# Optimization experiments

Measured on AMD Instinct MI355X. Metric: run time of the kernel, lower is better.

## Reference

```python
import jax, jax.numpy as jnp
import numpy as np

H = 12
PD = 4
DECAY = 0.99
OFFSETS = (1, 2, 4, 8)
_PI = np.array([0, 0, 0, 1, 1, 2])  # Plucker pair indices i for G(2,4)
_PJ = np.array([1, 2, 3, 2, 3, 3])  # Plucker pair indices j
_J6 = jnp.array([[0, 0, 0, 0, 0, 1], [0, 0, 0, 0, -1, 0], [0, 0, 0, 1, 0, 0],
                 [0, 0, 1, 0, 0, 0], [0, -1, 0, 0, 0, 0], [1, 0, 0, 0, 0, 0]],
                dtype=jnp.float32)


def exterior(p1, p2):
    # p1, p2: [..., 4] -> normalized Plucker coords [..., 6]
    L = p1[..., _PI] * p2[..., _PJ] - p1[..., _PJ] * p2[..., _PI]
    n = jnp.maximum(jnp.linalg.norm(L, axis=-1, keepdims=True), 1e-12)
    return L / n


def setup_inputs() -> dict:
    key = jax.random.key(0)
    ks = jax.random.split(key, 12)
    B, T, D = 2, 2048, 768
    s = 0.02
    return {
        "x": jax.random.normal(ks[0], (B, T, D), jnp.float32),
        "qkv_w": jax.random.normal(ks[1], (3 * D, D), jnp.float32) * s,
        "qkv_b": jnp.zeros((3 * D,), jnp.float32),
        "w1_write": jax.random.normal(ks[2], (PD * H, D), jnp.float32) * s,
        "w2_write": jax.random.normal(ks[3], (PD * H, D), jnp.float32) * s,
        "w1_read": jax.random.normal(ks[4], (PD * H, D), jnp.float32) * s,
        "w2_read": jax.random.normal(ks[5], (PD * H, D), jnp.float32) * s,
        "memv_w": jax.random.normal(ks[6], (D, D), jnp.float32) * s,
        "memv_b": jnp.zeros((D,), jnp.float32),
        "memg_w": jax.random.normal(ks[7], (H, D), jnp.float32) * s,
        "memg_b": jnp.zeros((H,), jnp.float32),
        "mem_scale": jnp.full((H,), 0.1, jnp.float32),
        "out_w": jax.random.normal(ks[8], (D, D), jnp.float32) * s,
        "out_b": jnp.zeros((D,), jnp.float32),
    }


def reference(x, qkv_w, qkv_b, w1_write, w2_write, w1_read, w2_read,
              memv_w, memv_b, memg_w, memg_b, mem_scale, out_w, out_b):
    B, T, D = x.shape
    dh = D // H
    scale = dh ** -0.5

    # --- standard causal attention (dropout disabled / eval mode) ---
    qkv = (x @ qkv_w.T + qkv_b).reshape(B, T, 3, H, dh)
    qkv = jnp.transpose(qkv, (2, 0, 3, 1, 4))  # [3,B,H,T,dh]
    q, k, v = qkv[0], qkv[1], qkv[2]
    att = jnp.einsum('bhtd,bhsd->bhts', q, k) * scale
    upper = jnp.triu(jnp.ones((T, T), bool), 1)
    att = jnp.where(upper, -jnp.inf, att)
    attn = jax.nn.softmax(att, axis=-1)
    seq_out = jnp.einsum('bhts,bhsd->bhtd', attn, v)
    seq_out = jnp.transpose(seq_out, (0, 2, 1, 3)).reshape(B, T, D)

    # --- multi-scale Plucker incidence memory ---
    r1 = (x @ w1_read.T).reshape(B, T, H, PD)
    r2 = (x @ w2_read.T).reshape(B, T, H, PD)
    read_h = jnp.transpose(exterior(r1, r2), (0, 2, 1, 3))  # [B,H,T,6]

    keep = jnp.tril(jnp.ones((T, T), bool), -1)  # strict lower triangle
    total = jnp.zeros((B, H, T, T), x.dtype)
    n_active = 0
    for off in OFFSETS:
        if off >= T:
            continue
        n_active += 1
        x_past = jnp.concatenate(
            [jnp.zeros((B, off, D), x.dtype), x[:, :-off]], axis=1)
        w1 = (x_past @ w1_write.T).reshape(B, T, H, PD)
        w2 = (x @ w2_write.T).reshape(B, T, H, PD)
        wl = exterior(w1, w2)                       # [B,T,H,6]
        jw = jnp.einsum('bthi,ij->bthj', wl, _J6)   # apply J
        jw = jnp.transpose(jw, (0, 2, 1, 3))        # [B,H,T,6]
        inc = jnp.einsum('bhtp,bhsp->bhts', read_h, jw)
        total = total + jnp.where(keep, inc * inc, 0.0)
    total = total / n_active

    pos = jnp.arange(T, dtype=x.dtype)
    decay_w = jnp.where(keep, DECAY ** (pos[:, None] - pos[None, :]), 0.0)
    total = total * decay_w
    mem_score = total.sum(axis=-1)  # [B,H,T]

    mem_val = x @ memv_w.T + memv_b
    gate = jax.nn.sigmoid(x @ memg_w.T + memg_b)  # [B,T,H]
    gated = jax.nn.sigmoid(jnp.transpose(mem_score, (0, 2, 1)) * mem_scale) * gate
    gated = gated.mean(axis=-1, keepdims=True)  # [B,T,1]

    return (seq_out + gated * mem_val) @ out_w.T + out_b
```

## Files before the change

### kernel.cpp

```cpp
#include <hip/hip_runtime.h>

#define H 12
#define T 2048
#define D 768
#define NBT 4096
#define SCALE 0.125f
#define DECAY_F 0.99f
#define NCHK 72
#define NBLK_ATTN (24 * NCHK)
#define NBLK_MS1 192

typedef __attribute__((ext_vector_type(8))) short bf16x8;
typedef __attribute__((ext_vector_type(4))) float f32x4;
typedef __attribute__((ext_vector_type(16))) float f32x16;

static __device__ __forceinline__ ushort f2bf(float f) {
  union { float f; unsigned u; } v; v.f = f;
  unsigned r = (v.u + 0x7FFFu + ((v.u >> 16) & 1u)) >> 16;
  return (ushort)r;
}
static __device__ __forceinline__ float bf2f(ushort u) {
  union { unsigned u; float f; } v; v.u = ((unsigned)u) << 16;
  return v.f;
}
static __device__ __forceinline__ unsigned cvtpk(float lo, float hi) {
  unsigned r;
  asm("v_cvt_pk_bf16_f32 %0, %1, %2" : "=v"(r) : "v"(lo), "v"(hi));
  return r;
}
static __device__ __forceinline__ void swap32(unsigned &a, unsigned &b) {
  asm("v_permlane32_swap_b32 %0, %1" : "+v"(a), "+v"(b));
}

static __device__ __forceinline__ void gload16(const void* g, void* s) {
  __builtin_amdgcn_global_load_lds(
      (const __attribute__((address_space(1))) unsigned int*)g,
      (__attribute__((address_space(3))) unsigned int*)s, 16, 0, 0);
}

__global__ __launch_bounds__(256) void cast_all(
    const float* __restrict__ x, const float* __restrict__ qkv_w,
    const float* __restrict__ memv_w, const float* __restrict__ out_w,
    const float* __restrict__ w1w, const float* __restrict__ w2w,
    const float* __restrict__ w1r, const float* __restrict__ w2r,
    const float* __restrict__ memg_w, ushort* __restrict__ dst)
{
  const size_t i8 = ((size_t)blockIdx.x * 256 + threadIdx.x) * 8;
  const float* src; size_t off;
  if      (i8 < 3145728) { src = x;      off = i8; }
  else if (i8 < 4915200) { src = qkv_w;  off = i8 - 3145728; }
  else if (i8 < 5505024) { src = memv_w; off = i8 - 4915200; }
  else if (i8 < 5541888) { src = w1w;    off = i8 - 5505024; }
  else if (i8 < 5578752) { src = w2w;    off = i8 - 5541888; }
  else if (i8 < 5615616) { src = w1r;    off = i8 - 5578752; }
  else if (i8 < 5652480) { src = w2r;    off = i8 - 5615616; }
  else if (i8 < 5661696) { src = memg_w; off = i8 - 5652480; }
  else if (i8 < 5701632) { *(uint4*)(dst + i8) = make_uint4(0, 0, 0, 0); return; }
  else                   { src = out_w;  off = i8 - 5701632; }
  const float4 a = *(const float4*)(src + off);
  const float4 b = *(const float4*)(src + off + 4);
  bf16x8 o;
  o[0] = (short)f2bf(a.x); o[1] = (short)f2bf(a.y);
  o[2] = (short)f2bf(a.z); o[3] = (short)f2bf(a.w);
  o[4] = (short)f2bf(b.x); o[5] = (short)f2bf(b.y);
  o[6] = (short)f2bf(b.z); o[7] = (short)f2bf(b.w);
  *(bf16x8*)(dst + i8) = o;
}

__global__ __launch_bounds__(512, 2) void gemm8_mega(
    const ushort* __restrict__ A, const ushort* __restrict__ W,
    const float* __restrict__ qkv_b, const float* __restrict__ memv_b,
    ushort* __restrict__ memvp, float* __restrict__ pw,
    float* __restrict__ pmemg,
    ushort* __restrict__ Qb, ushort* __restrict__ Kb, ushort* __restrict__ Vtb)
{
  __shared__ ushort lds[65536];
  const int tid = threadIdx.x;
  const int w = tid >> 6, l = tid & 63;
  const int wm = w >> 2, wn = w & 3;
  const int l15 = l & 15, l4 = l >> 4;

  int bid = blockIdx.x;
  bid = (bid & 7) * 26 + (bid >> 3);
  const int bx = bid % 13, by = bid / 13;
  const int bm = by * 256, bn = bx * 256;

  f32x4 acc[8][4];
#pragma unroll
  for (int i = 0; i < 8; i++)
#pragma unroll
    for (int j = 0; j < 4; j++) acc[i][j] = (f32x4){0.f, 0.f, 0.f, 0.f};

  auto stage = [&](int s, int isB, int h, int kt) {
    const ushort* src = (isB ? W + (size_t)bn * 768 : A + (size_t)bm * 768);
#pragma unroll
    for (int j = 0; j < 2; j++) {
      const int chunk = j * 512 + tid;
      const int r = chunk >> 3, c = chunk & 7;
      const int csrc = c ^ (r & 7);
      gload16(src + (size_t)(h * 128 + r) * 768 + kt * 64 + csrc * 8,
              (char*)lds + s * 65536 + isB * 32768 + h * 16384
                         + (size_t)(j * 512 + w * 64) * 16);
    }
  };
  auto rdA = [&](int s, int mi, int ks) -> bf16x8 {
    const int row = wm * 128 + mi * 16 + l15;
    const int ch = (ks * 4 + l4) ^ (l15 & 7);
    return *(const bf16x8*)((const char*)lds + s * 65536 + row * 128 + ch * 16);
  };
  auto rdB = [&](int s, int ni, int ks) -> bf16x8 {
    const int row = wn * 64 + ni * 16 + l15;
    const int ch = (ks * 4 + l4) ^ (l15 & 7);
    return *(const bf16x8*)((const char*)lds + s * 65536 + 32768 + row * 128 + ch * 16);
  };

  stage(0, 1, 0, 0); stage(0, 1, 1, 0); stage(0, 0, 0, 0); stage(0, 0, 1, 0);

#define MFMA_QUAD(mb, ks)                                                      \
  {                                                                            \
    __builtin_amdgcn_s_setprio(1);                                             \
    _Pragma("unroll")                                                          \
    for (int mi = 0; mi < 4; mi++) {                                           \
      const bf16x8 av = rdA(s, (mb) + mi, (ks));                               \
      acc[(mb)+mi][0] = __builtin_amdgcn_mfma_f32_16x16x32_bf16(av, bq0, acc[(mb)+mi][0], 0, 0, 0); \
      acc[(mb)+mi][1] = __builtin_amdgcn_mfma_f32_16x16x32_bf16(av, bq1, acc[(mb)+mi][1], 0, 0, 0); \
      acc[(mb)+mi][2] = __builtin_amdgcn_mfma_f32_16x16x32_bf16(av, bq2, acc[(mb)+mi][2], 0, 0, 0); \
      acc[(mb)+mi][3] = __builtin_amdgcn_mfma_f32_16x16x32_bf16(av, bq3, acc[(mb)+mi][3], 0, 0, 0); \
    }                                                                          \
    __builtin_amdgcn_s_setprio(0);                                             \
  }

  for (int t = 0; t < 12; t++) {
    const int s = t & 1, sn = s ^ 1;
    const int ktn = (t + 1) % 12;
    bf16x8 bq0, bq1, bq2, bq3;
    stage(sn, 1, 0, ktn);
    asm volatile("s_waitcnt vmcnt(2)" ::: "memory");
    __builtin_amdgcn_s_barrier();
    __builtin_amdgcn_sched_barrier(0);
    bq0 = rdB(s, 0, 0); bq1 = rdB(s, 1, 0); bq2 = rdB(s, 2, 0); bq3 = rdB(s, 3, 0);
    MFMA_QUAD(0, 0);
    __builtin_amdgcn_s_barrier();
    stage(sn, 1, 1, ktn);
    MFMA_QUAD(4, 0);
    __builtin_amdgcn_s_barrier();
    stage(sn, 0, 0, ktn);
    bq0 = rdB(s, 0, 1); bq1 = rdB(s, 1, 1); bq2 = rdB(s, 2, 1); bq3 = rdB(s, 3, 1);
    MFMA_QUAD(0, 1);
    __builtin_amdgcn_s_barrier();
    stage(sn, 0, 1, ktn);
    MFMA_QUAD(4, 1);
    __builtin_amdgcn_s_barrier();
  }

#pragma unroll
  for (int mi = 0; mi < 8; mi++) {
    const int row0 = bm + wm * 128 + mi * 16 + l4 * 4;
    const int b = row0 >> 11, tl = row0 & (T - 1);
#pragma unroll
    for (int ni = 0; ni < 4; ni++) {
      const int col = bn + wn * 64 + ni * 16 + l15;
      const f32x4 a4 = acc[mi][ni];
      if (col < 2304) {
        const float bv = qkv_b[col];
        const int sec = col / 768, cm = col % 768;
        const int h = cm >> 6, d = cm & 63;
        if (sec < 2) {
          ushort* dst = sec ? Kb : Qb;
#pragma unroll
          for (int r = 0; r < 4; r++)
            dst[((size_t)(b * H + h) * T + tl + r) * 64 + d] = f2bf(a4[r] + bv);
        } else {
          uint2 u;
          u.x = (unsigned)f2bf(a4[0] + bv) | ((unsigned)f2bf(a4[1] + bv) << 16);
          u.y = (unsigned)f2bf(a4[2] + bv) | ((unsigned)f2bf(a4[3] + bv) << 16);
          *(uint2*)(Vtb + ((size_t)(b * H + h) * 64 + d) * T + tl) = u;
        }
      } else if (col < 3072) {
        const int c2 = col - 2304;
        const float bv = memv_b[c2];
#pragma unroll
        for (int r = 0; r < 4; r++)
          memvp[(size_t)(row0 + r) * 768 + c2] = f2bf(a4[r] + bv);
      } else if (col < 3276) {
        const int c2 = col - 3072;
        if (c2 < 192) {
          float* pb = pw + (size_t)(c2 / 48) * (H * NBT * 4);
          const int hh = (c2 % 48) >> 2, comp = c2 & 3;
#pragma unroll
          for (int r = 0; r < 4; r++)
            pb[((size_t)hh * NBT + row0 + r) * 4 + comp] = a4[r];
        } else {
#pragma unroll
          for (int r = 0; r < 4; r++)
            pmemg[(size_t)(c2 - 192) * NBT + row0 + r] = a4[r];
        }
      }
    }
  }
}

__global__ __launch_bounds__(256) void gemm_out64(
    const ushort* __restrict__ A, const ushort* __restrict__ W,
    const float* __restrict__ bias, float* __restrict__ C)
{
  __shared__ ushort A_lds[128 * 64];
  __shared__ ushort B_lds[64 * 64];
  const int tid = threadIdx.x;
  const int w = tid >> 6, l = tid & 63;
  const int wm = w >> 1, wn = w & 1;
  const int bm = blockIdx.y * 128, bn = blockIdx.x * 64;
  const int l15 = l & 15, l4 = l >> 4;

  f32x4 acc[4][2];
#pragma unroll
  for (int i = 0; i < 4; i++)
#pragma unroll
    for (int j = 0; j < 2; j++) acc[i][j] = (f32x4){0.f, 0.f, 0.f, 0.f};

  const int srowA = w * 32 + (l >> 3);
  const int srowB = w * 16 + (l >> 3);
  const int scol = (l & 7) * 8;
  const ushort* Ag = A + (size_t)(bm + srowA) * 768 + scol;
  const ushort* Wg = W + (size_t)(bn + srowB) * 768 + scol;
  ushort* Asl = &A_lds[(w * 32) * 64];
  ushort* Bsl = &B_lds[(w * 16) * 64];

  for (int k0 = 0; k0 < 768; k0 += 64) {
#pragma unroll
    for (int i = 0; i < 4; i++)
      gload16(Ag + k0 + i * 8 * 768, Asl + i * 8 * 64);
#pragma unroll
    for (int i = 0; i < 2; i++)
      gload16(Wg + k0 + i * 8 * 768, Bsl + i * 8 * 64);
    __syncthreads();
#pragma unroll
    for (int ks = 0; ks < 2; ks++) {
      bf16x8 af[4], bfr[2];
#pragma unroll
      for (int i = 0; i < 4; i++)
        af[i] = *(const bf16x8*)&A_lds[(wm * 64 + i * 16 + l15) * 64 + ks * 32 + l4 * 8];
#pragma unroll
      for (int i = 0; i < 2; i++)
        bfr[i] = *(const bf16x8*)&B_lds[(wn * 32 + i * 16 + l15) * 64 + ks * 32 + l4 * 8];
#pragma unroll
      for (int mi = 0; mi < 4; mi++)
#pragma unroll
        for (int ni = 0; ni < 2; ni++)
          acc[mi][ni] = __builtin_amdgcn_mfma_f32_16x16x32_bf16(af[mi], bfr[ni], acc[mi][ni], 0, 0, 0);
    }
    __syncthreads();
  }
#pragma unroll
  for (int mi = 0; mi < 4; mi++) {
    const int row0 = bm + wm * 64 + mi * 16 + l4 * 4;
#pragma unroll
    for (int ni = 0; ni < 2; ni++) {
      const int col = bn + wn * 32 + ni * 16 + l15;
      const float bv = bias[col];
#pragma unroll
      for (int r = 0; r < 4; r++)
        C[(size_t)(row0 + r) * 768 + col] = acc[mi][ni][r] + bv;
    }
  }
}

__device__ __forceinline__ void ext_norm6(const float4 a, const float4 b, float* L)
{
  L[0] = a.x * b.y - a.y * b.x;
  L[1] = a.x * b.z - a.z * b.x;
  L[2] = a.x * b.w - a.w * b.x;
  L[3] = a.y * b.z - a.z * b.y;
  L[4] = a.y * b.w - a.w * b.y;
  L[5] = a.z * b.w - a.w * b.z;
  float n2 = L[0]*L[0] + L[1]*L[1] + L[2]*L[2] + L[3]*L[3] + L[4]*L[4] + L[5]*L[5];
  float n = fmaxf(sqrtf(n2), 1e-12f);
  float inv = 1.f / n;
#pragma unroll
  for (int i = 0; i < 6; i++) L[i] *= inv;
}

static __device__ void memscan1_body(
    int bb, char* smem, const float* __restrict__ pw,
    float* __restrict__ Rp, float* __restrict__ G)
{
  const int bh = bb >> 3, chunk = bb & 7;
  const int b = bh / H, h = bh % H;
  const int tid = threadIdx.x;
  float (*S)[22] = (float(*)[22])smem;
  const int t = chunk * 256 + tid;
  const size_t hb = (size_t)h * NBT + (size_t)b * T;
  const float* pw1w = pw + 0 * (size_t)(H * NBT * 4) + hb * 4;
  const float* pw2w = pw + 1 * (size_t)(H * NBT * 4) + hb * 4;
  const float* pw1r = pw + 2 * (size_t)(H * NBT * 4) + hb * 4;
  const float* pw2r = pw + 3 * (size_t)(H * NBT * 4) + hb * 4;

  float Cm[21];
#pragma unroll
  for (int c = 0; c < 21; c++) Cm[c] = 0.f;
  {
    const float4 w2 = *(const float4*)(pw2w + (size_t)t * 4);
    const int offs[4] = {1, 2, 4, 8};
#pragma unroll
    for (int oi = 0; oi < 4; oi++) {
      const int off = offs[oi];
      if (t >= off) {
        const float4 w1 = *(const float4*)(pw1w + (size_t)(t - off) * 4);
        float L[6];
        ext_norm6(w1, w2, L);
        const float Jv[6] = { L[5], -L[4], L[3], L[2], -L[1], L[0] };
        int c = 0;
#pragma unroll
        for (int p = 0; p < 6; p++)
#pragma unroll
          for (int q = p; q < 6; q++) { Cm[c] += Jv[p] * Jv[q]; c++; }
      }
    }
  }
  float R[6];
  {
    const float4 r1 = *(const float4*)(pw1r + (size_t)t * 4);
    const float4 r2 = *(const float4*)(pw2r + (size_t)t * 4);
    ext_norm6(r1, r2, R);
  }

#pragma unroll
  for (int c = 0; c < 21; c++) S[tid][c] = Cm[c];
  __syncthreads();
  float pd = DECAY_F;
  for (int off = 1; off < 256; off <<= 1) {
    float tmpv[21];
#pragma unroll
    for (int c = 0; c < 21; c++) tmpv[c] = (tid >= off) ? S[tid - off][c] : 0.f;
    __syncthreads();
#pragma unroll
    for (int c = 0; c < 21; c++) S[tid][c] += pd * tmpv[c];
    __syncthreads();
    pd *= pd;
  }
  float P[21];
#pragma unroll
  for (int c = 0; c < 21; c++) P[c] = (tid > 0) ? DECAY_F * S[tid - 1][c] : 0.f;

  float part1 = 0.f;
  {
    int c = 0;
#pragma unroll
    for (int p = 0; p < 6; p++) {
      part1 += P[c] * R[p] * R[p]; c++;
#pragma unroll
      for (int q = p + 1; q < 6; q++) { part1 += 2.f * P[c] * R[p] * R[q]; c++; }
    }
  }
  float* rp = Rp + ((size_t)bh * T + t) * 8;
  *(float4*)rp = make_float4(R[0], R[1], R[2], R[3]);
  *(float4*)(rp + 4) = make_float4(R[4], R[5], part1, 0.f);
  if (tid < 21)
    G[((size_t)bh * 8 + chunk) * 21 + tid] = S[255][tid];
}

__global__ __launch_bounds__(256) void attn_memscan(
    const ushort* __restrict__ Qb, const ushort* __restrict__ Kb,
    const ushort* __restrict__ Vtb, ushort* __restrict__ o_part,
    float* __restrict__ rs_part,
    const float* __restrict__ pw, float* __restrict__ Rp, float* __restrict__ G)
{
  __shared__ __align__(16) char smem[36864];

  if (blockIdx.x < NBLK_MS1) {
    memscan1_body(blockIdx.x, smem, pw, Rp, G);
    return;
  }
  const int abid = blockIdx.x - NBLK_MS1;

  typedef ushort row72[72];
  row72* K_lds = (row72*)smem;
  row72* V_lds = (row72*)(smem + 18432);

  const int bh = abid / NCHK;
  const int ci2 = 71 - (abid % NCHK);
  int ci = ci2;
  int qb = 15;
#pragma unroll
  for (int q = 0; q < 16; q++) {
    const int cnt = (q >> 1) + 1;
    if (ci < cnt) { qb = q; break; }
    ci -= cnt;
  }
  const int slot = bh * NCHK + ci2;
  const int t0 = qb * 128;
  const int it0 = ci * 4;
  const int it1 = min(it0 + 4, 2 * qb + 2);

  const int tid = threadIdx.x;
  const int w = tid >> 6;
  const int l = tid & 63;
  const int l31 = l & 31;
  const int lhi = l >> 5;

  bf16x8 qf[4];
  {
    const ushort* qp = Qb + ((size_t)bh * T + t0 + w * 32 + l31) * 64 + 8 * lhi;
#pragma unroll
    for (int kf = 0; kf < 4; kf++) qf[kf] = *(const bf16x8*)(qp + kf * 16);
  }
  f32x16 o0, o1;
#pragma unroll
  for (int r = 0; r < 16; r++) { o0[r] = 0.f; o1[r] = 0.f; }
  float rs = 0.f;

  const int sr = tid >> 2;
  const int scg = (tid & 3) * 16;
  const ushort* ksrc = Kb + ((size_t)bh * T + sr) * 64 + scg;
  const ushort* vsrc = Vtb + ((size_t)bh * 64 + sr) * T + scg;
  const int qlo = t0 + w * 32;
  const int qg = qlo + l31;

  bf16x8 kA0, kA1, vA0, vA1, kB0, kB1, vB0, vB1;
  {
    const size_t sa = (size_t)it0 * 64, sb = sa + 64;
    kA0 = *(const bf16x8*)(ksrc + sa * 64);
    kA1 = *(const bf16x8*)(ksrc + sa * 64 + 8);
    vA0 = *(const bf16x8*)(vsrc + sa);
    vA1 = *(const bf16x8*)(vsrc + sa + 8);
    kB0 = *(const bf16x8*)(ksrc + sb * 64);
    kB1 = *(const bf16x8*)(ksrc + sb * 64 + 8);
    vB0 = *(const bf16x8*)(vsrc + sb);
    vB1 = *(const bf16x8*)(vsrc + sb + 8);
  }

  auto process = [&](int s0, int ro) {
    f32x16 sA, sB;
#pragma unroll
    for (int r = 0; r < 16; r++) { sA[r] = 0.f; sB[r] = 0.f; }
    __builtin_amdgcn_s_setprio(1);
#pragma unroll
    for (int kf = 0; kf < 4; kf++) {
      const bf16x8 ka  = *(const bf16x8*)&K_lds[ro + l31][kf * 16 + 8 * lhi];
      const bf16x8 kb2 = *(const bf16x8*)&K_lds[ro + 32 + l31][kf * 16 + 8 * lhi];
      sA = __builtin_amdgcn_mfma_f32_32x32x16_bf16(ka, qf[kf], sA, 0, 0, 0);
      sB = __builtin_amdgcn_mfma_f32_32x32x16_bf16(kb2, qf[kf], sB, 0, 0, 0);
    }
    __builtin_amdgcn_s_setprio(0);

    const bool nomask = (s0 + 63 <= qlo);
#pragma unroll
    for (int half = 0; half < 2; half++) {
      float pv[16];
#pragma unroll
      for (int r = 0; r < 16; r++) {
        const int srow = (r & 3) + 8 * (r >> 2) + 4 * lhi;
        const float sv = (half == 0) ? sA[r] : sB[r];
        float p = __expf(sv * SCALE);
        if (!nomask && (s0 + half * 32 + srow > qg)) p = 0.f;
        rs += p;
        pv[r] = p;
      }
#pragma unroll
      for (int sub = 0; sub < 2; sub++) {
        const float* p8 = pv + 8 * sub;
        unsigned X = cvtpk(p8[0], p8[1]);
        unsigned Y = cvtpk(p8[4], p8[5]);
        unsigned Z = cvtpk(p8[2], p8[3]);
        unsigned Wd = cvtpk(p8[6], p8[7]);
        swap32(X, Y);
        swap32(Z, Wd);
        union { unsigned u[4]; bf16x8 v; } fr;
        fr.u[0] = X; fr.u[1] = Z; fr.u[2] = Y; fr.u[3] = Wd;
        const int ksl = half * 2 + sub;
        const bf16x8 va = *(const bf16x8*)&V_lds[ro + l31][ksl * 16 + 8 * lhi];
        const bf16x8 vb = *(const bf16x8*)&V_lds[ro + 32 + l31][ksl * 16 + 8 * lhi];
        __builtin_amdgcn_s_setprio(1);
        o0 = __builtin_amdgcn_mfma_f32_32x32x16_bf16(va, fr.v, o0, 0, 0, 0);
        o1 = __builtin_amdgcn_mfma_f32_32x32x16_bf16(vb, fr.v, o1, 0, 0, 0);
        __builtin_amdgcn_s_setprio(0);
      }
    }
  };

  for (int its = it0; its < it1; its += 2) {
    __syncthreads();
    *(bf16x8*)&K_lds[sr][scg]       = kA0;
    *(bf16x8*)&K_lds[sr][scg + 8]   = kA1;
    *(bf16x8*)&V_lds[sr][scg]       = vA0;
    *(bf16x8*)&V_lds[sr][scg + 8]   = vA1;
    *(bf16x8*)&K_lds[64 + sr][scg]     = kB0;
    *(bf16x8*)&K_lds[64 + sr][scg + 8] = kB1;
    *(bf16x8*)&V_lds[64 + sr][scg]     = vB0;
    *(bf16x8*)&V_lds[64 + sr][scg + 8] = vB1;
    __syncthreads();
    if (its + 2 < it1) {
      const size_t sa = (size_t)(its + 2) * 64, sb = sa + 64;
      kA0 = *(const bf16x8*)(ksrc + sa * 64);
      kA1 = *(const bf16x8*)(ksrc + sa * 64 + 8);
      vA0 = *(const bf16x8*)(vsrc + sa);
      vA1 = *(const bf16x8*)(vsrc + sa + 8);
      kB0 = *(const bf16x8*)(ksrc + sb * 64);
      kB1 = *(const bf16x8*)(ksrc + sb * 64 + 8);
      vB0 = *(const bf16x8*)(vsrc + sb);
      vB1 = *(const bf16x8*)(vsrc + sb + 8);
    }
    const int s0A = its * 64, s0B = s0A + 64;
    if (s0A <= qlo + 31) process(s0A, 0);
    if (s0B <= qlo + 31) process(s0B, 64);
  }

  rs += __shfl_xor(rs, 32);

  const int brow = w * 32 + l31;
  ushort* ob = o_part + ((size_t)slot * 128 + brow) * 64;
  float* rsb = rs_part + (size_t)slot * 128;
#pragma unroll
  for (int r = 0; r < 16; r += 2) {
    const int d = (r & 3) + 8 * (r >> 2) + 4 * lhi;
    *(unsigned*)(ob + d)      = cvtpk(o0[r], o0[r + 1]);
    *(unsigned*)(ob + 32 + d) = cvtpk(o1[r], o1[r + 1]);
  }
  if (l < 32) rsb[brow] = rs;
}

__global__ __launch_bounds__(256) void gatescan(
    const float* __restrict__ G, const float* __restrict__ Rp,
    const float* __restrict__ pmemg, const float* __restrict__ memg_b,
    const float* __restrict__ mem_scale, float* __restrict__ gate12)
{
  __shared__ float E[8][21];
  const int bh = blockIdx.x;
  const int b = bh / H, h = bh % H;
  const int tid = threadIdx.x;
  if (tid < 21) {
    float e = 0.f;
    const float d256 = 0.076314145f;
    for (int c = 0; c < 8; c++) {
      E[c][tid] = e;
      e = DECAY_F * G[((size_t)bh * 8 + c) * 21 + tid] + d256 * e;
    }
  }
  __syncthreads();
  const int chunk = tid >> 5;
  const int base = (tid & 31) * 8;
  float Ec[21];
#pragma unroll
  for (int c = 0; c < 21; c++) Ec[c] = E[chunk][c];

  const float msc = mem_scale[h];
  const float gb = memg_b[h];
  const size_t hb = (size_t)h * NBT + (size_t)b * T;
  const size_t rb = (size_t)b * T;
  float dj = __powf(DECAY_F, (float)base);
  for (int j = 0; j < 8; j++) {
    const int tl = chunk * 256 + base + j;
    const float* rp = Rp + ((size_t)bh * T + tl) * 8;
    const float4 q0 = *(const float4*)rp;
    const float4 q1 = *(const float4*)(rp + 4);
    const float R[6] = { q0.x, q0.y, q0.z, q0.w, q1.x, q1.y };
    const float part1 = q1.z;
    float qd = 0.f;
    {
      int c = 0;
#pragma unroll
      for (int p = 0; p < 6; p++) {
        qd += Ec[c] * R[p] * R[p]; c++;
#pragma unroll
        for (int q = p + 1; q < 6; q++) { qd += 2.f * Ec[c] * R[p] * R[q]; c++; }
      }
    }
    const float score = (part1 + dj * qd) * 0.25f;
    const float g1 = 1.f / (1.f + __expf(-score * msc));
    const float graw = pmemg[hb + tl] + gb;
    const float g2 = 1.f / (1.f + __expf(-graw));
    gate12[(rb + tl) * H + h] = g1 * g2;
    dj *= DECAY_F;
  }
}

__global__ __launch_bounds__(256) void reduce_fuse(
    const ushort* __restrict__ o_part, const float* __restrict__ rs_part,
    const ushort* __restrict__ memv, const float* __restrict__ gate12,
    ushort* __restrict__ zb)
{
  const int idx = blockIdx.x * 256 + threadIdx.x;
  const int row = idx / 96, c = (idx % 96) * 8;
  const int h = c >> 6, d0 = c & 63;
  const int b = row >> 11, tl = row & (T - 1);
  const int qb = tl >> 7, rloc = tl & 127;
  const int m = qb >> 1;
  const int cnt = m + 1;
  const int base = m * (m + 1) + (qb & 1) * (m + 1);
  const size_t bid0 = (size_t)(b * H + h) * NCHK + base;

  float o[8] = {0.f, 0.f, 0.f, 0.f, 0.f, 0.f, 0.f, 0.f};
  float rsum = 0.f;
  for (int ci = 0; ci < cnt; ci++) {
    const bf16x8 pv = *(const bf16x8*)(o_part + ((bid0 + ci) * 128 + rloc) * 64 + d0);
#pragma unroll
    for (int j = 0; j < 8; j++) o[j] += bf2f((ushort)pv[j]);
    rsum += rs_part[(bid0 + ci) * 128 + rloc];
  }
  const float inv = 1.f / rsum;

  const float* gp = gate12 + (size_t)row * H;
  float gs = 0.f;
#pragma unroll
  for (int j = 0; j < 12; j++) gs += gp[j];
  const float g = gs * (1.f / 12.f);

  const bf16x8 mv = *(const bf16x8*)(memv + (size_t)row * D + c);
  bf16x8 z;
#pragma unroll
  for (int j = 0; j < 8; j++)
    z[j] = (short)f2bf(o[j] * inv + g * bf2f((ushort)mv[j]));
  *(bf16x8*)(zb + (size_t)row * D + c) = z;
}

extern "C" void kernel_launch(void* const* d_in, const int* in_sizes, int n_in,
                              void* d_out, int out_size, void* d_ws, size_t ws_size,
                              hipStream_t stream)
{
  const float* x      = (const float*)d_in[0];
  const float* qkv_w  = (const float*)d_in[1];
  const float* qkv_b  = (const float*)d_in[2];
  const float* w1w    = (const float*)d_in[3];
  const float* w2w    = (const float*)d_in[4];
  const float* w1r    = (const float*)d_in[5];
  const float* w2r    = (const float*)d_in[6];
  const float* memv_w = (const float*)d_in[7];
  const float* memv_b = (const float*)d_in[8];
  const float* memg_w = (const float*)d_in[9];
  const float* memg_b = (const float*)d_in[10];
  const float* mem_scale = (const float*)d_in[11];
  const float* out_w  = (const float*)d_in[12];
  const float* out_b  = (const float*)d_in[13];
  float* out = (float*)d_out;

  float* ws    = (float*)d_ws;
  float* pw    = ws;
  float* pmemg = pw + (size_t)4 * H * NBT * 4;
  float* gate12 = pmemg + (size_t)H * NBT;
  float* rs_part = gate12 + (size_t)NBT * H;
  float* Rp    = rs_part + (size_t)NBLK_ATTN * 128;
  float* G     = Rp + (size_t)24 * T * 8;
  ushort* memv = (ushort*)(G + 24 * 8 * 21 + 24);
  ushort* Xb  = memv + (size_t)NBT * D;
  ushort* Wb  = Xb + (size_t)NBT * D;
  ushort* Qb  = Wb + (size_t)NBT * D;
  ushort* Kb  = Qb + (size_t)24 * T * 64;
  ushort* Vtb = Kb + (size_t)24 * T * 64;
  ushort* zb  = Vtb + (size_t)24 * T * 64;
  ushort* o_part = zb + (size_t)NBT * D;

  const ushort* W_out = Wb + (size_t)3328 * 768;

  dim3 blk(256);
  cast_all<<<dim3(3072), blk, 0, stream>>>(x, qkv_w, memv_w, out_w,
                                           w1w, w2w, w1r, w2r, memg_w, Xb);

  gemm8_mega<<<dim3(16 * 13), dim3(512), 0, stream>>>(
      Xb, Wb, qkv_b, memv_b, memv, pw, pmemg, Qb, Kb, Vtb);

  attn_memscan<<<dim3(NBLK_ATTN + NBLK_MS1), blk, 0, stream>>>(
      Qb, Kb, Vtb, o_part, rs_part, pw, Rp, G);

  gatescan<<<dim3(24), blk, 0, stream>>>(G, Rp, pmemg, memg_b, mem_scale, gate12);

  reduce_fuse<<<dim3(NBT * 96 / 256), blk, 0, stream>>>(o_part, rs_part, memv,
                                                        gate12, zb);
  gemm_out64<<<dim3(12, 32), blk, 0, stream>>>(zb, W_out, out_b, out);
}
```

Before: 123.3 us.

## Coarsen attention KV chunks, widen output GEMM tile, use exp2 softmax

Attention work is now split into chunks of up to 8 KV tiles instead of 4, so each (b,h) gets 40 partial blocks instead of 72. This reduces the partial-output traffic and the reduction loop in reduce_fuse, whose indexing is updated to match. The output GEMM tile grows from 128x64 to 128x128, which halves the grid and increases reuse per block but may leave CUs idle. The softmax exponent is computed with exp2f and a prescaled constant, and the row sum is accumulated into four independent partial sums to shorten the dependency chain.

```diff
diff --git a/kernel.cpp b/kernel.cpp
--- a/kernel.cpp
+++ b/kernel.cpp
@@ -6,9 +6,10 @@
 #define NBT 4096
 #define SCALE 0.125f
 #define DECAY_F 0.99f
-#define NCHK 72
+#define NCHK 40
 #define NBLK_ATTN (24 * NCHK)
 #define NBLK_MS1 192
+#define EXP2C 0.18033688011f
 
 typedef __attribute__((ext_vector_type(8))) short bf16x8;
 typedef __attribute__((ext_vector_type(4))) float f32x4;
@@ -200,53 +201,50 @@
   }
 }
 
-__global__ __launch_bounds__(256) void gemm_out64(
+__global__ __launch_bounds__(256) void gemm_mfma128(
     const ushort* __restrict__ A, const ushort* __restrict__ W,
-    const float* __restrict__ bias, float* __restrict__ C)
+    const float* __restrict__ bias, float* __restrict__ C, int ldc)
 {
   __shared__ ushort A_lds[128 * 64];
-  __shared__ ushort B_lds[64 * 64];
+  __shared__ ushort B_lds[128 * 64];
   const int tid = threadIdx.x;
   const int w = tid >> 6, l = tid & 63;
   const int wm = w >> 1, wn = w & 1;
-  const int bm = blockIdx.y * 128, bn = blockIdx.x * 64;
+  const int bm = blockIdx.y * 128, bn = blockIdx.x * 128;
   const int l15 = l & 15, l4 = l >> 4;
 
-  f32x4 acc[4][2];
+  f32x4 acc[4][4];
 #pragma unroll
   for (int i = 0; i < 4; i++)
 #pragma unroll
-    for (int j = 0; j < 2; j++) acc[i][j] = (f32x4){0.f, 0.f, 0.f, 0.f};
-
-  const int srowA = w * 32 + (l >> 3);
-  const int srowB = w * 16 + (l >> 3);
+    for (int j = 0; j < 4; j++) acc[i][j] = (f32x4){0.f, 0.f, 0.f, 0.f};
+
+  const int srow = w * 32 + (l >> 3);
   const int scol = (l & 7) * 8;
-  const ushort* Ag = A + (size_t)(bm + srowA) * 768 + scol;
-  const ushort* Wg = W + (size_t)(bn + srowB) * 768 + scol;
+  const ushort* Ag = A + (size_t)(bm + srow) * 768 + scol;
+  const ushort* Wg = W + (size_t)(bn + srow) * 768 + scol;
   ushort* Asl = &A_lds[(w * 32) * 64];
-  ushort* Bsl = &B_lds[(w * 16) * 64];
+  ushort* Bsl = &B_lds[(w * 32) * 64];
 
   for (int k0 = 0; k0 < 768; k0 += 64) {
 #pragma unroll
-    for (int i = 0; i < 4; i++)
+    for (int i = 0; i < 4; i++) {
       gload16(Ag + k0 + i * 8 * 768, Asl + i * 8 * 64);
-#pragma unroll
-    for (int i = 0; i < 2; i++)
       gload16(Wg + k0 + i * 8 * 768, Bsl + i * 8 * 64);
+    }
     __syncthreads();
 #pragma unroll
     for (int ks = 0; ks < 2; ks++) {
-      bf16x8 af[4], bfr[2];
-#pragma unroll
-      for (int i = 0; i < 4; i++)
-        af[i] = *(const bf16x8*)&A_lds[(wm * 64 + i * 16 + l15) * 64 + ks * 32 + l4 * 8];
-#pragma unroll
-      for (int i = 0; i < 2; i++)
-        bfr[i] = *(const bf16x8*)&B_lds[(wn * 32 + i * 16 + l15) * 64 + ks * 32 + l4 * 8];
+      bf16x8 af[4], bfr[4];
+#pragma unroll
+      for (int i = 0; i < 4; i++) {
+        af[i]  = *(const bf16x8*)&A_lds[(wm * 64 + i * 16 + l15) * 64 + ks * 32 + l4 * 8];
+        bfr[i] = *(const bf16x8*)&B_lds[(wn * 64 + i * 16 + l15) * 64 + ks * 32 + l4 * 8];
+      }
 #pragma unroll
       for (int mi = 0; mi < 4; mi++)
 #pragma unroll
-        for (int ni = 0; ni < 2; ni++)
+        for (int ni = 0; ni < 4; ni++)
           acc[mi][ni] = __builtin_amdgcn_mfma_f32_16x16x32_bf16(af[mi], bfr[ni], acc[mi][ni], 0, 0, 0);
     }
     __syncthreads();
@@ -255,12 +253,12 @@
   for (int mi = 0; mi < 4; mi++) {
     const int row0 = bm + wm * 64 + mi * 16 + l4 * 4;
 #pragma unroll
-    for (int ni = 0; ni < 2; ni++) {
-      const int col = bn + wn * 32 + ni * 16 + l15;
+    for (int ni = 0; ni < 4; ni++) {
+      const int col = bn + wn * 64 + ni * 16 + l15;
       const float bv = bias[col];
 #pragma unroll
       for (int r = 0; r < 4; r++)
-        C[(size_t)(row0 + r) * 768 + col] = acc[mi][ni][r] + bv;
+        C[(size_t)(row0 + r) * ldc + col] = acc[mi][ni][r] + bv;
     }
   }
 }
@@ -378,19 +376,19 @@
   row72* V_lds = (row72*)(smem + 18432);
 
   const int bh = abid / NCHK;
-  const int ci2 = 71 - (abid % NCHK);
+  const int ci2 = (NCHK - 1) - (abid % NCHK);
   int ci = ci2;
   int qb = 15;
 #pragma unroll
   for (int q = 0; q < 16; q++) {
-    const int cnt = (q >> 1) + 1;
+    const int cnt = (q >> 2) + 1;
     if (ci < cnt) { qb = q; break; }
     ci -= cnt;
   }
   const int slot = bh * NCHK + ci2;
   const int t0 = qb * 128;
-  const int it0 = ci * 4;
-  const int it1 = min(it0 + 4, 2 * qb + 2);
+  const int it0 = ci * 8;
+  const int it1 = min(it0 + 8, 2 * qb + 2);
 
   const int tid = threadIdx.x;
   const int w = tid >> 6;
@@ -407,7 +405,7 @@
   f32x16 o0, o1;
 #pragma unroll
   for (int r = 0; r < 16; r++) { o0[r] = 0.f; o1[r] = 0.f; }
-  float rs = 0.f;
+  float rs0 = 0.f, rs1 = 0.f, rs2 = 0.f, rs3 = 0.f;
 
   const int sr = tid >> 2;
   const int scg = (tid & 3) * 16;
@@ -451,11 +449,14 @@
       for (int r = 0; r < 16; r++) {
         const int srow = (r & 3) + 8 * (r >> 2) + 4 * lhi;
         const float sv = (half == 0) ? sA[r] : sB[r];
-        float p = __expf(sv * SCALE);
+        float p = exp2f(sv * EXP2C);
         if (!nomask && (s0 + half * 32 + srow > qg)) p = 0.f;
-        rs += p;
         pv[r] = p;
       }
+      rs0 += pv[0] + pv[1];  rs1 += pv[2] + pv[3];
+      rs2 += pv[4] + pv[5];  rs3 += pv[6] + pv[7];
+      rs0 += pv[8] + pv[9];  rs1 += pv[10] + pv[11];
+      rs2 += pv[12] + pv[13]; rs3 += pv[14] + pv[15];
 #pragma unroll
       for (int sub = 0; sub < 2; sub++) {
         const float* p8 = pv + 8 * sub;
@@ -505,6 +506,7 @@
     if (s0B <= qlo + 31) process(s0B, 64);
   }
 
+  float rs = (rs0 + rs1) + (rs2 + rs3);
   rs += __shfl_xor(rs, 32);
 
   const int brow = w * 32 + l31;
@@ -584,9 +586,9 @@
   const int h = c >> 6, d0 = c & 63;
   const int b = row >> 11, tl = row & (T - 1);
   const int qb = tl >> 7, rloc = tl & 127;
-  const int m = qb >> 1;
-  const int cnt = m + 1;
-  const int base = m * (m + 1) + (qb & 1) * (m + 1);
+  const int g = qb >> 2;
+  const int cnt = g + 1;
+  const int base = 2 * g * (g + 1) + (qb & 3) * (g + 1);
   const size_t bid0 = (size_t)(b * H + h) * NCHK + base;
 
   float o[8] = {0.f, 0.f, 0.f, 0.f, 0.f, 0.f, 0.f, 0.f};
@@ -603,13 +605,13 @@
   float gs = 0.f;
 #pragma unroll
   for (int j = 0; j < 12; j++) gs += gp[j];
-  const float g = gs * (1.f / 12.f);
+  const float gt = gs * (1.f / 12.f);
 
   const bf16x8 mv = *(const bf16x8*)(memv + (size_t)row * D + c);
   bf16x8 z;
 #pragma unroll
   for (int j = 0; j < 8; j++)
-    z[j] = (short)f2bf(o[j] * inv + g * bf2f((ushort)mv[j]));
+    z[j] = (short)f2bf(o[j] * inv + gt * bf2f((ushort)mv[j]));
   *(bf16x8*)(zb + (size_t)row * D + c) = z;
 }
 
@@ -658,12 +660,12 @@
   gemm8_mega<<<dim3(16 * 13), dim3(512), 0, stream>>>(
       Xb, Wb, qkv_b, memv_b, memv, pw, pmemg, Qb, Kb, Vtb);
 
-  attn_memscan<<<dim3(NBLK_ATTN + NBLK_MS1), blk, 0, stream>>>(
+  attn_memscan<<<dim3(NBLK_MS1 + NBLK_ATTN), blk, 0, stream>>>(
       Qb, Kb, Vtb, o_part, rs_part, pw, Rp, G);
 
   gatescan<<<dim3(24), blk, 0, stream>>>(G, Rp, pmemg, memg_b, mem_scale, gate12);
 
   reduce_fuse<<<dim3(NBT * 96 / 256), blk, 0, stream>>>(o_part, rs_part, memv,
                                                         gate12, zb);
-  gemm_out64<<<dim3(12, 32), blk, 0, stream>>>(zb, W_out, out_b, out);
-}
+  gemm_mfma128<<<dim3(6, 32), blk, 0, stream>>>(zb, W_out, out_b, out, 768);
+}
```

New measurement: 128.6 us. 4.3% more time.
